# Kernel optimization log

Hardware: AMD Instinct MI355X
Metric: run time of the kernel (lower is better)

Reference implementation:

```python
import jax, jax.numpy as jnp
import numpy as np
jax.config.update("jax_enable_x64", True)

T_OLD = 60000
T_NEW = 60000
NV = 30000
MAX_STEPS = 300
FB_CHUNK = 500  # T_OLD must be divisible by this

FACE_OPP = np.array([[1, 2, 3], [0, 2, 3], [0, 1, 3], [0, 1, 2]])
EDGES = [(0, 1), (0, 2), (0, 3), (1, 2), (1, 3), (2, 3)]


def setup_inputs() -> dict:
    key = jax.random.key(0)
    k1, k2, k3, k4, k5 = jax.random.split(key, 5)
    # distinct vertices per tet (sorted base + strictly increasing offsets)
    off = jnp.arange(4, dtype=jnp.int64)
    new_indices = jnp.sort(jax.random.randint(k1, (T_NEW, 4), 0, NV - 4, dtype=jnp.int64), axis=1) + off
    old_indices = jnp.sort(jax.random.randint(k2, (T_OLD, 4), 0, NV - 4, dtype=jnp.int64), axis=1) + off
    return {
        "new_indices": new_indices,
        "old_indices": old_indices,
        "old_cc": jax.random.normal(k3, (T_OLD, 3), dtype=jnp.float32),
        "new_cc": jax.random.normal(k4, (T_NEW, 3), dtype=jnp.float32),
        "vertex_positions": jax.random.uniform(k5, (NV, 3), dtype=jnp.float32),
    }


def _min_edge_length(verts, indices):
    p = verts[indices]  # (T,4,3)
    el = jnp.stack([jnp.linalg.norm(p[:, a] - p[:, b], axis=-1) for a, b in EDGES])
    return el.min(axis=0)


def _forward(new_indices, old_indices, old_cc, new_cc, vertex_positions):
    T_new = new_indices.shape[0]
    T_old = old_indices.shape[0]
    Vn = vertex_positions.shape[0]

    # --- 1. unchanged-tet detection via sorted-vertex int64 keys ---
    key4 = lambda s: ((s[:, 0] * Vn + s[:, 1]) * Vn + s[:, 2]) * Vn + s[:, 3]
    ok = key4(jnp.sort(old_indices, axis=1))
    nk = key4(jnp.sort(new_indices, axis=1))
    order = jnp.argsort(ok)
    sk = ok[order]
    pos = jnp.searchsorted(sk, nk, side='right') - 1
    posc = jnp.clip(pos, 0, T_old - 1)
    matched = jnp.where((pos >= 0) & (sk[posc] == nk), order[posc], -1)
    is_matched = matched >= 0
    matched_safe = jnp.maximum(matched, 0)

    # --- 2. face adjacency of old mesh (sorted face keys, adjacent-equal pairing) ---
    fi = jnp.sort(old_indices[:, FACE_OPP], axis=2)          # (T_old,4,3)
    fk = (fi[..., 0] * Vn + fi[..., 1]) * Vn + fi[..., 2]    # (T_old,4)
    all_keys = fk.T.reshape(-1)                              # f-major like the numpy concat
    all_tets = jnp.tile(jnp.arange(T_old), 4)
    all_locals = jnp.repeat(jnp.arange(4), T_old)
    o2 = jnp.argsort(all_keys)
    sk2, st, sl = all_keys[o2], all_tets[o2], all_locals[o2]
    same = sk2[:-1] == sk2[1:]
    neighbors = jnp.full((T_old, 4), -1, dtype=jnp.int64)
    neighbors = neighbors.at[jnp.where(same, st[:-1], T_old), sl[:-1]].set(st[1:], mode='drop')
    neighbors = neighbors.at[jnp.where(same, st[1:], T_old), sl[1:]].set(st[:-1], mode='drop')

    # --- 3. per-old-tet inverse edge matrix; degenerate tets get no neighbors ---
    verts = jax.lax.stop_gradient(vertex_positions).astype(jnp.float32)
    p = verts[old_indices]                                   # (T_old,4,3)
    v0 = p[:, 0]
    Tm = jnp.stack([p[:, 1] - v0, p[:, 2] - v0, p[:, 3] - v0], axis=-1)
    degen = jnp.abs(jnp.linalg.det(Tm)) < 1e-10
    Tinv = jnp.linalg.inv(jnp.where(degen[:, None, None], jnp.eye(3, dtype=Tm.dtype), Tm))
    neighbors = jnp.where(degen[:, None], -1, neighbors)

    prio = jnp.full((Vn,), -1, dtype=jnp.int64)
    ar = jnp.arange(T_old)
    for vi in range(4):
        prio = prio.at[old_indices[:, vi]].max(vi * T_old + ar)
    v2t = jnp.where(prio >= 0, prio % T_old, 0)

    # --- 5. barycentric walk (masked, all float inputs stop-gradiented; int outputs) ---
    cent = jax.lax.stop_gradient(verts[new_indices].mean(axis=1))  # (T_new,3)
    seed = v2t[new_indices[:, 0]]
    n_walk = jnp.sum(~is_matched)
    thr = jnp.maximum(jnp.int64(100), n_walk // 1000)

    def cond(state):
        step, cur, rem, act = state
        return (step < MAX_STEPS) & (jnp.sum(act) >= thr)

    def body(state):
        step, cur, rem, act = state
        rel = cent - v0[cur]
        bary = jnp.einsum('nij,nj->ni', Tinv[cur], rel)
        all_b = jnp.concatenate([(1.0 - bary.sum(axis=1))[:, None], bary], axis=1)
        conv = act & (all_b.min(axis=1) >= -1e-4)
        rem = jnp.where(conv, cur, rem)
        act = act & ~conv
        nb = neighbors[cur, jnp.argmin(all_b, axis=1)]
        at_bd = act & (nb < 0)
        rem = jnp.where(at_bd, cur, rem)
        act = act & ~at_bd
        cur = jnp.where(act, nb, cur)
        return (step + 1, cur, rem, act)

    _, cur, rem, act = jax.lax.while_loop(cond, body, (jnp.int64(0), seed, seed, ~is_matched))
    rem = jnp.where(act, cur, rem)

    # --- 6. nearest-centroid fallback for unfinished walks (gated, chunked) ---
    old_cents = jax.lax.stop_gradient(verts[old_indices].mean(axis=1))

    def fallback(_):
        p2 = (cent ** 2).sum(-1)
        c2 = (old_cents ** 2).sum(-1)
        def scan_body(carry, i):
            bd, bi = carry
            c = jax.lax.dynamic_slice(old_cents, (i * FB_CHUNK, 0), (FB_CHUNK, 3))
            cn = jax.lax.dynamic_slice(c2, (i * FB_CHUNK,), (FB_CHUNK,))
            d = p2[:, None] - 2.0 * (cent @ c.T) + cn[None, :]
            md = d.min(axis=1)
            mi = d.argmin(axis=1).astype(jnp.int64) + i * FB_CHUNK
            imp = md < bd
            return (jnp.where(imp, md, bd), jnp.where(imp, mi, bi)), None
        init = (jnp.full((T_new,), jnp.inf, dtype=jnp.float32), jnp.zeros((T_new,), dtype=jnp.int64))
        (bd, bi), _ = jax.lax.scan(scan_body, init, jnp.arange(T_old // FB_CHUNK))
        return bi

    fb = jax.lax.cond(jnp.sum(act) > 0, fallback, lambda _: jnp.zeros((T_new,), dtype=jnp.int64), None)
    rem = jnp.clip(jnp.where(act, fb, rem), 0, T_old - 1)
    remap = jnp.where(is_matched, matched_safe, rem)

    # --- 7. candidates: containing tet + 4 face neighbors ---
    face_nb = neighbors[remap]
    face_nb = jnp.where(face_nb >= 0, face_nb, remap[:, None])
    cands = jnp.concatenate([remap[:, None], face_nb], axis=1)            # (T_new,5)
    cands = jnp.where(is_matched[:, None], matched_safe[:, None], cands)

    # --- 8. overlap / circumcenter-distance weights ---
    cand_verts = old_indices[cands]                                       # (T_new,5,4)
    overlap = (cand_verts[:, :, :, None] == new_indices[:, None, None, :]).any(-1).sum(-1).astype(jnp.float32)
    cc_d2 = ((old_cc[cands] - new_cc[:, None, :]) ** 2).sum(-1)
    raw = jnp.exp(overlap * 2.0) / (cc_d2 + 1e-8)
    weights = raw / raw.sum(axis=1, keepdims=True)

    # --- 9. density scale: min-edge-length ratio ---
    old_el = _min_edge_length(vertex_positions, old_indices)[cands]
    new_el = _min_edge_length(vertex_positions, new_indices)
    density_scale = jnp.clip(old_el / jnp.maximum(new_el[:, None], 1e-8), 0.1, 10.0)

    return cands, weights, density_scale


_forward_jit = jax.jit(_forward)


def reference(new_indices, old_indices, old_cc, new_cc, vertex_positions):
    return _forward_jit(new_indices, old_indices, old_cc, new_cc, vertex_positions)
```

## Files before the change

kernel.cpp:

```cpp
#include <hip/hip_runtime.h>

#pragma clang fp contract(off)

#define TOLD 60000
#define TNEW 60000
#define NVERT 30000
#define MAXSTEPS 300
#define THSZ 131072
#define FHSZ 131072
#define EMPTY64 0xFFFFFFFFFFFFFFFFULL
#define NWGR 60
#define VRANGE 500
#define NSLICE 16
#define TSLICE (TOLD / NSLICE)

#define NB_SETUP 235
#define NB_PRIO  (NWGR * NSLICE)
#define NB_NEWG  235
#define NB_FACE  938
#define NB_FOLD  118
#define NB_MATCH 235
#define NB_FB    120
#define FBRANGE  (TNEW / NB_FB)

#define OFF_TKEYS    0u
#define OFF_FTAB     1048576u
#define OFF_NBR      2097152u
#define FF_BYTES     3057152u
#define OFF_CNT      3057152u
#define OFF_TVALS    3059200u
#define OFF_PPRIO    3583488u
#define OFF_PRIO     5503488u
#define OFF_IDXOLD   5623488u
#define OFF_SSTEP    6583488u
#define OFF_DEGEN    6823488u
#define OFF_MATCHED  7063488u
#define OFF_TV4      7303488u
#define OFF_COLD4    10183488u
#define OFF_CNEW4    11143488u
#define OFF_DM       12103488u

struct P {
  const unsigned int* rawNew;
  const unsigned int* rawOld;
  const float* occ;
  const float* ncc;
  const float* verts;
  float* out;
  unsigned long long* tkeys;
  unsigned long long* ftab;
  int* counters;
  int* tvals;
  int* idxOld;
  int* nbr;
  int* pprio;
  int* prio;
  int* sstep;
  int* degen;
  int* matched;
  float4* Tv4;
  float4* cold4;
  float4* cnew4;
  unsigned long long* dm;
  unsigned int dmMask;
};

__device__ __forceinline__ unsigned hash64(unsigned long long k){
  k ^= k >> 33; k *= 0xff51afd7ed558ccdULL;
  k ^= k >> 33; k *= 0xc4ceb9fe1a85ec53ULL;
  k ^= k >> 33;
  return (unsigned)k;
}
__device__ __forceinline__ void cswap(int& a, int& b){ if (a > b){ int t = a; a = b; b = t; } }

__device__ __forceinline__ int detect64(const unsigned int* raw){
  unsigned acc = 0;
  const uint4* r4 = (const uint4*)raw;
  #pragma unroll
  for (int k = 0; k < 32; ++k){ uint4 v = r4[k]; acc |= (v.y | v.w); }
  return acc == 0u;
}

__device__ __forceinline__ int4 load_tet4(const unsigned int* raw, int is64, int t){
  if (is64){
    uint4 a = ((const uint4*)raw)[t * 2 + 0];
    uint4 b = ((const uint4*)raw)[t * 2 + 1];
    return make_int4((int)a.x, (int)a.z, (int)b.x, (int)b.z);
  }
  uint4 a = ((const uint4*)raw)[t];
  return make_int4((int)a.x, (int)a.y, (int)a.z, (int)a.w);
}

__device__ __forceinline__ void face_insert(unsigned long long* ftab, int* nbr,
                                            unsigned long long fkey, int t, int l){
  unsigned long long mine = (fkey << 18) | (unsigned long long)(t * 4 + l);
  unsigned slot = hash64(fkey ^ 0x9e3779b97f4a7c15ULL) & (FHSZ - 1);
  while (true){
    unsigned long long prev = atomicCAS(&ftab[slot], EMPTY64, mine);
    if (prev == EMPTY64) return;
    if ((prev >> 18) == fkey){
      int oid = (int)(prev & 0x3FFFFULL);
      nbr[t * 4 + l] = oid >> 2;
      nbr[oid] = t;
      return;
    }
    slot = (slot + 1) & (FHSZ - 1);
  }
}

__device__ __forceinline__ float min_edge_r(
    float q0x, float q0y, float q0z, float q1x, float q1y, float q1z,
    float q2x, float q2y, float q2z, float q3x, float q3y, float q3z){
  float m = 3.402823466e+38f;
  float dx, dy, dz, d;
  dx = q0x - q1x; dy = q0y - q1y; dz = q0z - q1z; d = sqrtf((dx*dx + dy*dy) + dz*dz); m = fminf(m, d);
  dx = q0x - q2x; dy = q0y - q2y; dz = q0z - q2z; d = sqrtf((dx*dx + dy*dy) + dz*dz); m = fminf(m, d);
  dx = q0x - q3x; dy = q0y - q3y; dz = q0z - q3z; d = sqrtf((dx*dx + dy*dy) + dz*dz); m = fminf(m, d);
  dx = q1x - q2x; dy = q1y - q2y; dz = q1z - q2z; d = sqrtf((dx*dx + dy*dy) + dz*dz); m = fminf(m, d);
  dx = q1x - q3x; dy = q1y - q3y; dz = q1z - q3z; d = sqrtf((dx*dx + dy*dy) + dz*dz); m = fminf(m, d);
  dx = q2x - q3x; dy = q2y - q3y; dz = q2z - q3z; d = sqrtf((dx*dx + dy*dy) + dz*dz); m = fminf(m, d);
  return m;
}

__global__ __launch_bounds__(256) void k_front(P p){
  __shared__ int sprio[VRANGE];
  int bb = blockIdx.x;
  if (bb < NB_SETUP){
    int t = bb * 256 + threadIdx.x;
    if (bb == 0){
      for (int j = threadIdx.x; j < 384; j += 256) p.counters[j] = 0;
    }
    if (t >= TOLD) return;
    int is64 = detect64(p.rawOld);
    int4 iv4 = load_tet4(p.rawOld, is64, t);
    int i0 = iv4.x, i1 = iv4.y, i2 = iv4.z, i3 = iv4.w;
    ((int4*)p.idxOld)[t] = iv4;

    {
      int s0 = i0, s1 = i1, s2 = i2, s3 = i3;
      cswap(s0, s1); cswap(s2, s3); cswap(s0, s2); cswap(s1, s3); cswap(s1, s2);
      unsigned long long key =
          (unsigned long long)((((long long)s0 * NVERT + s1) * NVERT + s2) * NVERT + s3);
      unsigned slot = hash64(key) & (THSZ - 1);
      while (true){
        unsigned long long prev = atomicCAS(&p.tkeys[slot], EMPTY64, key);
        if (prev == EMPTY64){ p.tvals[slot] = t; break; }
        if (prev == key){ atomicMax(&p.tvals[slot], t); break; }
        slot = (slot + 1) & (THSZ - 1);
      }
    }

    if (p.dmMask){
      const int FO[4][3] = {{1, 2, 3}, {0, 2, 3}, {0, 1, 3}, {0, 1, 2}};
      int iv[4] = {i0, i1, i2, i3};
      #pragma unroll
      for (int l = 0; l < 4; ++l){
        int a = iv[FO[l][0]], b = iv[FO[l][1]], c = iv[FO[l][2]];
        cswap(a, b); cswap(a, c); cswap(b, c);
        unsigned long long fk = (unsigned long long)(((long long)a * NVERT + b) * NVERT + c);
        p.dm[hash64(fk) & p.dmMask] = (fk << 18) | (unsigned long long)(t * 4 + l);
      }
    }

    float q0x = p.verts[i0 * 3 + 0], q0y = p.verts[i0 * 3 + 1], q0z = p.verts[i0 * 3 + 2];
    float q1x = p.verts[i1 * 3 + 0], q1y = p.verts[i1 * 3 + 1], q1z = p.verts[i1 * 3 + 2];
    float q2x = p.verts[i2 * 3 + 0], q2y = p.verts[i2 * 3 + 1], q2z = p.verts[i2 * 3 + 2];
    float q3x = p.verts[i3 * 3 + 0], q3y = p.verts[i3 * 3 + 1], q3z = p.verts[i3 * 3 + 2];
    float e1x = q1x - q0x, e1y = q1y - q0y, e1z = q1z - q0z;
    float e2x = q2x - q0x, e2y = q2y - q0y, e2z = q2z - q0z;
    float e3x = q3x - q0x, e3y = q3y - q0y, e3z = q3z - q0z;
    float c23x = e2y * e3z - e2z * e3y;
    float c23y = e2z * e3x - e2x * e3z;
    float c23z = e2x * e3y - e2y * e3x;
    float det = e1x * c23x + e1y * c23y + e1z * c23z;
    int dg = (fabsf(det) < 1e-10f) ? 1 : 0;
    p.degen[t] = dg;
    float4 r0, r1, r2;
    if (dg){
      r0 = make_float4(1.f, 0.f, 0.f, q0x);
      r1 = make_float4(0.f, 1.f, 0.f, q0y);
      r2 = make_float4(0.f, 0.f, 1.f, q0z);
    } else {
      float inv = 1.0f / det;
      float c31x = e3y * e1z - e3z * e1y;
      float c31y = e3z * e1x - e3x * e1z;
      float c31z = e3x * e1y - e3y * e1x;
      float c12x = e1y * e2z - e1z * e2y;
      float c12y = e1z * e2x - e1x * e2z;
      float c12z = e1x * e2y - e1y * e2x;
      r0 = make_float4(c23x * inv, c23y * inv, c23z * inv, q0x);
      r1 = make_float4(c31x * inv, c31y * inv, c31z * inv, q0y);
      r2 = make_float4(c12x * inv, c12y * inv, c12z * inv, q0z);
    }
    p.Tv4[t * 3 + 0] = r0;
    p.Tv4[t * 3 + 1] = r1;
    p.Tv4[t * 3 + 2] = r2;
    float el = min_edge_r(q0x, q0y, q0z, q1x, q1y, q1z, q2x, q2y, q2z, q3x, q3y, q3z);
    p.cold4[t] = make_float4((((q0x + q1x) + q2x) + q3x) * 0.25f,
                             (((q0y + q1y) + q2y) + q3y) * 0.25f,
                             (((q0z + q1z) + q2z) + q3z) * 0.25f, el);
  } else if (bb < NB_SETUP + NB_PRIO){
    int rb = bb - NB_SETUP;
    int range = rb / NSLICE;
    int slice = rb % NSLICE;
    int base = range * VRANGE;
    for (int j = threadIdx.x; j < VRANGE; j += 256) sprio[j] = -1;
    __syncthreads();
    int is64 = detect64(p.rawOld);
    int t0 = slice * TSLICE;
    for (int t = t0 + threadIdx.x; t < t0 + TSLICE; t += 256){
      int4 iv = load_tet4(p.rawOld, is64, t);
      int v;
      v = iv.x - base; if ((unsigned)v < VRANGE) atomicMax(&sprio[v], 0 * TOLD + t);
      v = iv.y - base; if ((unsigned)v < VRANGE) atomicMax(&sprio[v], 1 * TOLD + t);
      v = iv.z - base; if ((unsigned)v < VRANGE) atomicMax(&sprio[v], 2 * TOLD + t);
      v = iv.w - base; if ((unsigned)v < VRANGE) atomicMax(&sprio[v], 3 * TOLD + t);
    }
    __syncthreads();
    for (int j = threadIdx.x; j < VRANGE; j += 256)
      p.pprio[slice * NVERT + base + j] = sprio[j];
  } else {
    int n = (bb - NB_SETUP - NB_PRIO) * 256 + threadIdx.x;
    if (n >= TNEW) return;
    int is64 = detect64(p.rawNew);
    int4 ni = load_tet4(p.rawNew, is64, n);
    float q0x = p.verts[ni.x * 3 + 0], q0y = p.verts[ni.x * 3 + 1], q0z = p.verts[ni.x * 3 + 2];
    float q1x = p.verts[ni.y * 3 + 0], q1y = p.verts[ni.y * 3 + 1], q1z = p.verts[ni.y * 3 + 2];
    float q2x = p.verts[ni.z * 3 + 0], q2y = p.verts[ni.z * 3 + 1], q2z = p.verts[ni.z * 3 + 2];
    float q3x = p.verts[ni.w * 3 + 0], q3y = p.verts[ni.w * 3 + 1], q3z = p.verts[ni.w * 3 + 2];
    float el = min_edge_r(q0x, q0y, q0z, q1x, q1y, q1z, q2x, q2y, q2z, q3x, q3y, q3z);
    p.cnew4[n] = make_float4((((q0x + q1x) + q2x) + q3x) * 0.25f,
                             (((q0y + q1y) + q2y) + q3y) * 0.25f,
                             (((q0z + q1z) + q2z) + q3z) * 0.25f, el);
  }
}

__global__ __launch_bounds__(256) void k_mid(P p){
  int bb = blockIdx.x;
  if (bb < NB_FACE){
    int i = bb * 256 + threadIdx.x;
    if (i >= TOLD * 4) return;
    int t = i >> 2, l = i & 3;
    int4 iv4 = ((const int4*)p.idxOld)[t];
    int iv[4] = {iv4.x, iv4.y, iv4.z, iv4.w};
    const int FO[4][3] = {{1, 2, 3}, {0, 2, 3}, {0, 1, 3}, {0, 1, 2}};
    int a = iv[FO[l][0]], b = iv[FO[l][1]], c = iv[FO[l][2]];
    cswap(a, b); cswap(a, c); cswap(b, c);
    unsigned long long fk = (unsigned long long)(((long long)a * NVERT + b) * NVERT + c);
    if (p.dmMask){
      unsigned long long mine = (fk << 18) | (unsigned long long)i;
      unsigned long long got = p.dm[hash64(fk) & p.dmMask];
      if (got == mine) return;
      if ((got >> 18) == fk){
        int wid = (int)(got & 0x3FFFFULL);
        p.nbr[i] = wid >> 2;
        p.nbr[wid] = t;
        return;
      }
    }
    face_insert(p.ftab, p.nbr, fk, t, l);
  } else if (bb < NB_FACE + NB_FOLD){
    int v = (bb - NB_FACE) * 256 + threadIdx.x;
    if (v >= NVERT) return;
    int pr = -1;
    #pragma unroll
    for (int s = 0; s < NSLICE; ++s) pr = max(pr, p.pprio[s * NVERT + v]);
    p.prio[v] = pr;
  } else {
    int n = (bb - NB_FACE - NB_FOLD) * 256 + threadIdx.x;
    if (n >= TNEW) return;
    int is64 = detect64(p.rawNew);
    int4 ni = load_tet4(p.rawNew, is64, n);
    int s0 = ni.x, s1 = ni.y, s2 = ni.z, s3 = ni.w;
    cswap(s0, s1); cswap(s2, s3); cswap(s0, s2); cswap(s1, s3); cswap(s1, s2);
    unsigned long long key =
        (unsigned long long)((((long long)s0 * NVERT + s1) * NVERT + s2) * NVERT + s3);
    int m = -1;
    unsigned slot = hash64(key) & (THSZ - 1);
    while (true){
      unsigned long long k = p.tkeys[slot];
      if (k == EMPTY64) break;
      if (k == key){ m = p.tvals[slot]; break; }
      slot = (slot + 1) & (THSZ - 1);
    }
    p.matched[n] = m;
  }
}

__device__ __forceinline__ void assemble_walker(const P& p, int n, int m, int remap){
  int cds[5];
  if (m >= 0){
    cds[0] = cds[1] = cds[2] = cds[3] = cds[4] = m;
  } else {
    cds[0] = remap;
    int dg = p.degen[remap];
    int4 nb4 = ((const int4*)p.nbr)[remap];
    int nbl[4] = {nb4.x, nb4.y, nb4.z, nb4.w};
    for (int l = 0; l < 4; ++l){
      int fb = dg ? -1 : nbl[l];
      cds[1 + l] = (fb >= 0) ? fb : remap;
    }
  }
  bool same = (cds[1] == cds[0]) & (cds[2] == cds[0]) &
              (cds[3] == cds[0]) & (cds[4] == cds[0]);
  int is64 = detect64(p.rawNew);
  int4 ni = load_tet4(p.rawNew, is64, n);
  float nc0 = p.ncc[n * 3 + 0], nc1 = p.ncc[n * 3 + 1], nc2 = p.ncc[n * 3 + 2];
  float nelv = fmaxf(p.cnew4[n].w, 1e-8f);
  if (same){
    int ct = cds[0];
    int4 cv = ((const int4*)p.idxOld)[ct];
    int ov = 0;
    ov += (cv.x == ni.x || cv.x == ni.y || cv.x == ni.z || cv.x == ni.w) ? 1 : 0;
    ov += (cv.y == ni.x || cv.y == ni.y || cv.y == ni.z || cv.y == ni.w) ? 1 : 0;
    ov += (cv.z == ni.x || cv.z == ni.y || cv.z == ni.z || cv.z == ni.w) ? 1 : 0;
    ov += (cv.w == ni.x || cv.w == ni.y || cv.w == ni.z || cv.w == ni.w) ? 1 : 0;
    float d0 = p.occ[ct * 3 + 0] - nc0;
    float d1 = p.occ[ct * 3 + 1] - nc1;
    float d2 = p.occ[ct * 3 + 2] - nc2;
    float ccd2 = (d0 * d0 + d1 * d1) + d2 * d2;
    float raw = expf((float)ov * 2.0f) / (ccd2 + 1e-8f);
    float rsum = 0.0f;
    rsum += raw; rsum += raw; rsum += raw; rsum += raw; rsum += raw;
    float wgt = raw / rsum;
    float ds = p.cold4[ct].w / nelv;
    ds = fminf(fmaxf(ds, 0.1f), 10.0f);
    float cf = (float)ct;
    for (int c = 0; c < 5; ++c){
      p.out[n * 5 + c] = cf;
      p.out[TNEW * 5 + n * 5 + c] = wgt;
      p.out[2 * TNEW * 5 + n * 5 + c] = ds;
    }
    return;
  }
  float raws[5]; float rsum = 0.0f;
  float oels[5];
  for (int c = 0; c < 5; ++c){
    int ct = cds[c];
    int4 cv = ((const int4*)p.idxOld)[ct];
    int ov = 0;
    ov += (cv.x == ni.x || cv.x == ni.y || cv.x == ni.z || cv.x == ni.w) ? 1 : 0;
    ov += (cv.y == ni.x || cv.y == ni.y || cv.y == ni.z || cv.y == ni.w) ? 1 : 0;
    ov += (cv.z == ni.x || cv.z == ni.y || cv.z == ni.z || cv.z == ni.w) ? 1 : 0;
    ov += (cv.w == ni.x || cv.w == ni.y || cv.w == ni.z || cv.w == ni.w) ? 1 : 0;
    float d0 = p.occ[ct * 3 + 0] - nc0;
    float d1 = p.occ[ct * 3 + 1] - nc1;
    float d2 = p.occ[ct * 3 + 2] - nc2;
    float ccd2 = (d0 * d0 + d1 * d1) + d2 * d2;
    float raw = expf((float)ov * 2.0f) / (ccd2 + 1e-8f);
    raws[c] = raw; rsum += raw;
    oels[c] = p.cold4[ct].w;
  }
  for (int c = 0; c < 5; ++c){
    p.out[n * 5 + c] = (float)cds[c];
    p.out[TNEW * 5 + n * 5 + c] = raws[c] / rsum;
    float ds = oels[c] / nelv;
    ds = fminf(fmaxf(ds, 0.1f), 10.0f);
    p.out[2 * TNEW * 5 + n * 5 + c] = ds;
  }
}

__global__ __launch_bounds__(256) void k_walkall(P p){
  __shared__ int s_hist[MAXSTEPS + 2];
  __shared__ int s_nw;
  for (int j = threadIdx.x; j < MAXSTEPS + 2; j += 256) s_hist[j] = 0;
  if (threadIdx.x == 0) s_nw = 0;
  __syncthreads();
  int n = blockIdx.x * blockDim.x + threadIdx.x;
  if (n < TNEW){
    int m = p.matched[n];
    if (m >= 0){
      assemble_walker(p, n, m, 0);
    } else {
      atomicAdd(&s_nw, 1);
      int is64 = detect64(p.rawNew);
      int i0 = is64 ? (int)((const long long*)p.rawNew)[n * 4] : ((const int*)p.rawNew)[n * 4];
      int pr = p.prio[i0];
      int c = (pr >= 0) ? (pr % TOLD) : 0;
      float4 cn = p.cnew4[n];
      int s = MAXSTEPS + 1;
      for (int k = 1; k <= MAXSTEPS; ++k){
        float4 r0 = p.Tv4[c * 3 + 0];
        float4 r1 = p.Tv4[c * 3 + 1];
        float4 r2 = p.Tv4[c * 3 + 2];
        float rx = cn.x - r0.w, ry = cn.y - r1.w, rz = cn.z - r2.w;
        float b0 = r0.x * rx + r0.y * ry + r0.z * rz;
        float b1 = r1.x * rx + r1.y * ry + r1.z * rz;
        float b2 = r2.x * rx + r2.y * ry + r2.z * rz;
        float a0 = 1.0f - (b0 + b1 + b2);
        float ab[4] = {a0, b0, b1, b2};
        int amin = 0; float mn = ab[0];
        for (int j = 1; j < 4; ++j){ if (ab[j] < mn){ mn = ab[j]; amin = j; } }
        if (mn >= -0.0001f){ s = k; break; }
        int nb = p.degen[c] ? -1 : p.nbr[c * 4 + amin];
        if (nb < 0){ s = k; break; }
        c = nb;
      }
      p.sstep[n] = s;
      atomicAdd(&s_hist[s], 1);
      assemble_walker(p, n, -1, c);
    }
  }
  __syncthreads();
  if (threadIdx.x == 0 && s_nw) atomicAdd(&p.counters[0], s_nw);
  for (int j = threadIdx.x; j < MAXSTEPS + 2; j += 256){
    int v = s_hist[j];
    if (v) atomicAdd(&p.counters[64 + j], v);
  }
}

__device__ __forceinline__ int compute_S(const int* counters){
  int nw = counters[0];
  int thr = max(100, nw / 1000);
  if (nw < thr) return 0;
  int cnt = nw;
  for (int k = 1; k <= MAXSTEPS; ++k){
    cnt -= counters[64 + k];
    if (cnt < thr) return k;
  }
  return MAXSTEPS;
}

__global__ __launch_bounds__(256) void k_tail(P p){
  __shared__ float sd[256];
  __shared__ int si[256];
  __shared__ int s_hits[256];
  __shared__ int s_nhits;
  __shared__ int s_S;
  if (threadIdx.x == 0) s_S = compute_S(p.counters);
  __syncthreads();
  int S = s_S;
  int base = blockIdx.x * FBRANGE;
  for (int chunk = base; chunk < base + FBRANGE; chunk += 256){
    if (threadIdx.x == 0) s_nhits = 0;
    __syncthreads();
    int n = chunk + threadIdx.x;
    if (n < base + FBRANGE && n < TNEW){
      if (p.matched[n] < 0 && p.sstep[n] > S)
        s_hits[atomicAdd(&s_nhits, 1)] = n;
    }
    __syncthreads();
    int nh = s_nhits;
    for (int h = 0; h < nh; ++h){
      int n2 = s_hits[h];
      float4 cn = p.cnew4[n2];
      float cx = cn.x, cy = cn.y, cz = cn.z;
      float p2 = (cx * cx + cy * cy) + cz * cz;
      float bd = 3.402823466e+38f; int bi = 0;
      for (int j = threadIdx.x; j < TOLD; j += 256){
        float4 oc = p.cold4[j];
        float dot = (cx * oc.x + cy * oc.y) + cz * oc.z;
        float c2 = (oc.x * oc.x + oc.y * oc.y) + oc.z * oc.z;
        float d = (p2 - 2.0f * dot) + c2;
        if (d < bd || (d == bd && j < bi)){ bd = d; bi = j; }
      }
      sd[threadIdx.x] = bd; si[threadIdx.x] = bi;
      __syncthreads();
      for (int s = 128; s > 0; s >>= 1){
        if ((int)threadIdx.x < s){
          float od = sd[threadIdx.x + s]; int oi = si[threadIdx.x + s];
          if (od < sd[threadIdx.x] || (od == sd[threadIdx.x] && oi < si[threadIdx.x])){
            sd[threadIdx.x] = od; si[threadIdx.x] = oi;
          }
        }
        __syncthreads();
      }
      if (threadIdx.x == 0){
        int r = si[0];
        if (r < 0) r = 0; if (r > TOLD - 1) r = TOLD - 1;
        assemble_walker(p, n2, -1, r);
      }
      __syncthreads();
    }
    __syncthreads();
  }
}

extern "C" void kernel_launch(void* const* d_in, const int* in_sizes, int n_in,
                              void* d_out, int out_size, void* d_ws, size_t ws_size,
                              hipStream_t stream) {
  char* w = (char*)d_ws;
  P p;
  p.rawNew = (const unsigned int*)d_in[0];
  p.rawOld = (const unsigned int*)d_in[1];
  p.occ    = (const float*)d_in[2];
  p.ncc    = (const float*)d_in[3];
  p.verts  = (const float*)d_in[4];
  p.out    = (float*)d_out;
  p.tkeys    = (unsigned long long*)(w + OFF_TKEYS);
  p.ftab     = (unsigned long long*)(w + OFF_FTAB);
  p.nbr      = (int*)(w + OFF_NBR);
  p.counters = (int*)(w + OFF_CNT);
  p.tvals    = (int*)(w + OFF_TVALS);
  p.pprio    = (int*)(w + OFF_PPRIO);
  p.prio     = (int*)(w + OFF_PRIO);
  p.idxOld   = (int*)(w + OFF_IDXOLD);
  p.sstep    = (int*)(w + OFF_SSTEP);
  p.degen    = (int*)(w + OFF_DEGEN);
  p.matched  = (int*)(w + OFF_MATCHED);
  p.Tv4      = (float4*)(w + OFF_TV4);
  p.cold4    = (float4*)(w + OFF_COLD4);
  p.cnew4    = (float4*)(w + OFF_CNEW4);
  p.dm       = (unsigned long long*)(w + OFF_DM);
  size_t avail = (ws_size > (size_t)OFF_DM) ? ws_size - (size_t)OFF_DM : 0;
  unsigned dmMask = 0;
  for (int bshift = 21; bshift >= 16; --bshift){
    if (avail >= ((size_t)8 << bshift)){ dmMask = (1u << bshift) - 1u; break; }
  }
  p.dmMask = dmMask;

  hipMemsetAsync(w, 0xFF, FF_BYTES, stream);
  hipLaunchKernelGGL(k_front,   dim3(NB_SETUP + NB_PRIO + NB_NEWG), dim3(256), 0, stream, p);
  hipLaunchKernelGGL(k_mid,     dim3(NB_FACE + NB_FOLD + NB_MATCH), dim3(256), 0, stream, p);
  hipLaunchKernelGGL(k_walkall, dim3((TNEW + 255) / 256), dim3(256), 0, stream, p);
  hipLaunchKernelGGL(k_tail,    dim3(NB_FB), dim3(256), 0, stream, p);
}
```

Before: 113.7 us.

## Fuse pipeline kernels into one persistent kernel with software grid barriers

Replaces the four separate launches (front, mid, walk, tail) with a single persistent kernel of 768 blocks. The blocks move between phases through an atomic-counter grid barrier that lives in the memset workspace. The per-vertex priority is now built with direct global atomicMax during setup, which removes the sliced LDS pass and the fold pass. The goal is to cut launch gaps and inter-kernel drain time, at the cost of barrier spin overhead, more contention on global atomics, and a deadlock risk if not all 768 blocks are resident at once.

```diff
diff --git a/kernel.cpp b/kernel.cpp
--- a/kernel.cpp
+++ b/kernel.cpp
@@ -9,16 +9,12 @@
 #define THSZ 131072
 #define FHSZ 131072
 #define EMPTY64 0xFFFFFFFFFFFFFFFFULL
-#define NWGR 60
-#define VRANGE 500
-#define NSLICE 16
-#define TSLICE (TOLD / NSLICE)
+
+#define GRID_NB 768
 
 #define NB_SETUP 235
-#define NB_PRIO  (NWGR * NSLICE)
 #define NB_NEWG  235
 #define NB_FACE  938
-#define NB_FOLD  118
 #define NB_MATCH 235
 #define NB_FB    120
 #define FBRANGE  (TNEW / NB_FB)
@@ -26,19 +22,19 @@
 #define OFF_TKEYS    0u
 #define OFF_FTAB     1048576u
 #define OFF_NBR      2097152u
-#define FF_BYTES     3057152u
-#define OFF_CNT      3057152u
-#define OFF_TVALS    3059200u
-#define OFF_PPRIO    3583488u
-#define OFF_PRIO     5503488u
-#define OFF_IDXOLD   5623488u
-#define OFF_SSTEP    6583488u
-#define OFF_DEGEN    6823488u
-#define OFF_MATCHED  7063488u
-#define OFF_TV4      7303488u
-#define OFF_COLD4    10183488u
-#define OFF_CNEW4    11143488u
-#define OFF_DM       12103488u
+#define OFF_PRIO     3057152u
+#define OFF_BAR      3177152u
+#define FF_BYTES     3177216u
+#define OFF_CNT      3177216u
+#define OFF_TVALS    3179264u
+#define OFF_IDXOLD   3703552u
+#define OFF_SSTEP    4663552u
+#define OFF_DEGEN    4903552u
+#define OFF_MATCHED  5143552u
+#define OFF_TV4      5383552u
+#define OFF_COLD4    8263552u
+#define OFF_CNEW4    9223552u
+#define OFF_DM       10183552u
 
 struct P {
   const unsigned int* rawNew;
@@ -53,7 +49,6 @@
   int* tvals;
   int* idxOld;
   int* nbr;
-  int* pprio;
   int* prio;
   int* sstep;
   int* degen;
@@ -62,6 +57,7 @@
   float4* cold4;
   float4* cnew4;
   unsigned long long* dm;
+  int* bar;
   unsigned int dmMask;
 };
 
@@ -122,169 +118,24 @@
   return m;
 }
 
-__global__ __launch_bounds__(256) void k_front(P p){
-  __shared__ int sprio[VRANGE];
-  int bb = blockIdx.x;
-  if (bb < NB_SETUP){
-    int t = bb * 256 + threadIdx.x;
-    if (bb == 0){
-      for (int j = threadIdx.x; j < 384; j += 256) p.counters[j] = 0;
-    }
-    if (t >= TOLD) return;
-    int is64 = detect64(p.rawOld);
-    int4 iv4 = load_tet4(p.rawOld, is64, t);
-    int i0 = iv4.x, i1 = iv4.y, i2 = iv4.z, i3 = iv4.w;
-    ((int4*)p.idxOld)[t] = iv4;
-
-    {
-      int s0 = i0, s1 = i1, s2 = i2, s3 = i3;
-      cswap(s0, s1); cswap(s2, s3); cswap(s0, s2); cswap(s1, s3); cswap(s1, s2);
-      unsigned long long key =
-          (unsigned long long)((((long long)s0 * NVERT + s1) * NVERT + s2) * NVERT + s3);
-      unsigned slot = hash64(key) & (THSZ - 1);
-      while (true){
-        unsigned long long prev = atomicCAS(&p.tkeys[slot], EMPTY64, key);
-        if (prev == EMPTY64){ p.tvals[slot] = t; break; }
-        if (prev == key){ atomicMax(&p.tvals[slot], t); break; }
-        slot = (slot + 1) & (THSZ - 1);
-      }
-    }
-
-    if (p.dmMask){
-      const int FO[4][3] = {{1, 2, 3}, {0, 2, 3}, {0, 1, 3}, {0, 1, 2}};
-      int iv[4] = {i0, i1, i2, i3};
-      #pragma unroll
-      for (int l = 0; l < 4; ++l){
-        int a = iv[FO[l][0]], b = iv[FO[l][1]], c = iv[FO[l][2]];
-        cswap(a, b); cswap(a, c); cswap(b, c);
-        unsigned long long fk = (unsigned long long)(((long long)a * NVERT + b) * NVERT + c);
-        p.dm[hash64(fk) & p.dmMask] = (fk << 18) | (unsigned long long)(t * 4 + l);
-      }
-    }
-
-    float q0x = p.verts[i0 * 3 + 0], q0y = p.verts[i0 * 3 + 1], q0z = p.verts[i0 * 3 + 2];
-    float q1x = p.verts[i1 * 3 + 0], q1y = p.verts[i1 * 3 + 1], q1z = p.verts[i1 * 3 + 2];
-    float q2x = p.verts[i2 * 3 + 0], q2y = p.verts[i2 * 3 + 1], q2z = p.verts[i2 * 3 + 2];
-    float q3x = p.verts[i3 * 3 + 0], q3y = p.verts[i3 * 3 + 1], q3z = p.verts[i3 * 3 + 2];
-    float e1x = q1x - q0x, e1y = q1y - q0y, e1z = q1z - q0z;
-    float e2x = q2x - q0x, e2y = q2y - q0y, e2z = q2z - q0z;
-    float e3x = q3x - q0x, e3y = q3y - q0y, e3z = q3z - q0z;
-    float c23x = e2y * e3z - e2z * e3y;
-    float c23y = e2z * e3x - e2x * e3z;
-    float c23z = e2x * e3y - e2y * e3x;
-    float det = e1x * c23x + e1y * c23y + e1z * c23z;
-    int dg = (fabsf(det) < 1e-10f) ? 1 : 0;
-    p.degen[t] = dg;
-    float4 r0, r1, r2;
-    if (dg){
-      r0 = make_float4(1.f, 0.f, 0.f, q0x);
-      r1 = make_float4(0.f, 1.f, 0.f, q0y);
-      r2 = make_float4(0.f, 0.f, 1.f, q0z);
+__device__ __forceinline__ void gridbar(int* bar){
+  __syncthreads();
+  if (threadIdx.x == 0){
+    __threadfence();
+    int g = __hip_atomic_load(&bar[1], __ATOMIC_ACQUIRE, __HIP_MEMORY_SCOPE_AGENT);
+    int v = __hip_atomic_fetch_add(&bar[0], 1, __ATOMIC_ACQ_REL, __HIP_MEMORY_SCOPE_AGENT);
+    if (v == GRID_NB - 2){
+      __hip_atomic_fetch_add(&bar[0], -GRID_NB, __ATOMIC_RELAXED, __HIP_MEMORY_SCOPE_AGENT);
+      __threadfence();
+      __hip_atomic_fetch_add(&bar[1], 1, __ATOMIC_RELEASE, __HIP_MEMORY_SCOPE_AGENT);
     } else {
-      float inv = 1.0f / det;
-      float c31x = e3y * e1z - e3z * e1y;
-      float c31y = e3z * e1x - e3x * e1z;
-      float c31z = e3x * e1y - e3y * e1x;
-      float c12x = e1y * e2z - e1z * e2y;
-      float c12y = e1z * e2x - e1x * e2z;
-      float c12z = e1x * e2y - e1y * e2x;
-      r0 = make_float4(c23x * inv, c23y * inv, c23z * inv, q0x);
-      r1 = make_float4(c31x * inv, c31y * inv, c31z * inv, q0y);
-      r2 = make_float4(c12x * inv, c12y * inv, c12z * inv, q0z);
-    }
-    p.Tv4[t * 3 + 0] = r0;
-    p.Tv4[t * 3 + 1] = r1;
-    p.Tv4[t * 3 + 2] = r2;
-    float el = min_edge_r(q0x, q0y, q0z, q1x, q1y, q1z, q2x, q2y, q2z, q3x, q3y, q3z);
-    p.cold4[t] = make_float4((((q0x + q1x) + q2x) + q3x) * 0.25f,
-                             (((q0y + q1y) + q2y) + q3y) * 0.25f,
-                             (((q0z + q1z) + q2z) + q3z) * 0.25f, el);
-  } else if (bb < NB_SETUP + NB_PRIO){
-    int rb = bb - NB_SETUP;
-    int range = rb / NSLICE;
-    int slice = rb % NSLICE;
-    int base = range * VRANGE;
-    for (int j = threadIdx.x; j < VRANGE; j += 256) sprio[j] = -1;
-    __syncthreads();
-    int is64 = detect64(p.rawOld);
-    int t0 = slice * TSLICE;
-    for (int t = t0 + threadIdx.x; t < t0 + TSLICE; t += 256){
-      int4 iv = load_tet4(p.rawOld, is64, t);
-      int v;
-      v = iv.x - base; if ((unsigned)v < VRANGE) atomicMax(&sprio[v], 0 * TOLD + t);
-      v = iv.y - base; if ((unsigned)v < VRANGE) atomicMax(&sprio[v], 1 * TOLD + t);
-      v = iv.z - base; if ((unsigned)v < VRANGE) atomicMax(&sprio[v], 2 * TOLD + t);
-      v = iv.w - base; if ((unsigned)v < VRANGE) atomicMax(&sprio[v], 3 * TOLD + t);
-    }
-    __syncthreads();
-    for (int j = threadIdx.x; j < VRANGE; j += 256)
-      p.pprio[slice * NVERT + base + j] = sprio[j];
-  } else {
-    int n = (bb - NB_SETUP - NB_PRIO) * 256 + threadIdx.x;
-    if (n >= TNEW) return;
-    int is64 = detect64(p.rawNew);
-    int4 ni = load_tet4(p.rawNew, is64, n);
-    float q0x = p.verts[ni.x * 3 + 0], q0y = p.verts[ni.x * 3 + 1], q0z = p.verts[ni.x * 3 + 2];
-    float q1x = p.verts[ni.y * 3 + 0], q1y = p.verts[ni.y * 3 + 1], q1z = p.verts[ni.y * 3 + 2];
-    float q2x = p.verts[ni.z * 3 + 0], q2y = p.verts[ni.z * 3 + 1], q2z = p.verts[ni.z * 3 + 2];
-    float q3x = p.verts[ni.w * 3 + 0], q3y = p.verts[ni.w * 3 + 1], q3z = p.verts[ni.w * 3 + 2];
-    float el = min_edge_r(q0x, q0y, q0z, q1x, q1y, q1z, q2x, q2y, q2z, q3x, q3y, q3z);
-    p.cnew4[n] = make_float4((((q0x + q1x) + q2x) + q3x) * 0.25f,
-                             (((q0y + q1y) + q2y) + q3y) * 0.25f,
-                             (((q0z + q1z) + q2z) + q3z) * 0.25f, el);
-  }
-}
-
-__global__ __launch_bounds__(256) void k_mid(P p){
-  int bb = blockIdx.x;
-  if (bb < NB_FACE){
-    int i = bb * 256 + threadIdx.x;
-    if (i >= TOLD * 4) return;
-    int t = i >> 2, l = i & 3;
-    int4 iv4 = ((const int4*)p.idxOld)[t];
-    int iv[4] = {iv4.x, iv4.y, iv4.z, iv4.w};
-    const int FO[4][3] = {{1, 2, 3}, {0, 2, 3}, {0, 1, 3}, {0, 1, 2}};
-    int a = iv[FO[l][0]], b = iv[FO[l][1]], c = iv[FO[l][2]];
-    cswap(a, b); cswap(a, c); cswap(b, c);
-    unsigned long long fk = (unsigned long long)(((long long)a * NVERT + b) * NVERT + c);
-    if (p.dmMask){
-      unsigned long long mine = (fk << 18) | (unsigned long long)i;
-      unsigned long long got = p.dm[hash64(fk) & p.dmMask];
-      if (got == mine) return;
-      if ((got >> 18) == fk){
-        int wid = (int)(got & 0x3FFFFULL);
-        p.nbr[i] = wid >> 2;
-        p.nbr[wid] = t;
-        return;
-      }
-    }
-    face_insert(p.ftab, p.nbr, fk, t, l);
-  } else if (bb < NB_FACE + NB_FOLD){
-    int v = (bb - NB_FACE) * 256 + threadIdx.x;
-    if (v >= NVERT) return;
-    int pr = -1;
-    #pragma unroll
-    for (int s = 0; s < NSLICE; ++s) pr = max(pr, p.pprio[s * NVERT + v]);
-    p.prio[v] = pr;
-  } else {
-    int n = (bb - NB_FACE - NB_FOLD) * 256 + threadIdx.x;
-    if (n >= TNEW) return;
-    int is64 = detect64(p.rawNew);
-    int4 ni = load_tet4(p.rawNew, is64, n);
-    int s0 = ni.x, s1 = ni.y, s2 = ni.z, s3 = ni.w;
-    cswap(s0, s1); cswap(s2, s3); cswap(s0, s2); cswap(s1, s3); cswap(s1, s2);
-    unsigned long long key =
-        (unsigned long long)((((long long)s0 * NVERT + s1) * NVERT + s2) * NVERT + s3);
-    int m = -1;
-    unsigned slot = hash64(key) & (THSZ - 1);
-    while (true){
-      unsigned long long k = p.tkeys[slot];
-      if (k == EMPTY64) break;
-      if (k == key){ m = p.tvals[slot]; break; }
-      slot = (slot + 1) & (THSZ - 1);
-    }
-    p.matched[n] = m;
-  }
+      while (__hip_atomic_load(&bar[1], __ATOMIC_RELAXED, __HIP_MEMORY_SCOPE_AGENT) == g){
+        __builtin_amdgcn_s_sleep(1);
+      }
+    }
+    __threadfence();
+  }
+  __syncthreads();
 }
 
 __device__ __forceinline__ void assemble_walker(const P& p, int n, int m, int remap){
@@ -360,55 +211,6 @@
   }
 }
 
-__global__ __launch_bounds__(256) void k_walkall(P p){
-  __shared__ int s_hist[MAXSTEPS + 2];
-  __shared__ int s_nw;
-  for (int j = threadIdx.x; j < MAXSTEPS + 2; j += 256) s_hist[j] = 0;
-  if (threadIdx.x == 0) s_nw = 0;
-  __syncthreads();
-  int n = blockIdx.x * blockDim.x + threadIdx.x;
-  if (n < TNEW){
-    int m = p.matched[n];
-    if (m >= 0){
-      assemble_walker(p, n, m, 0);
-    } else {
-      atomicAdd(&s_nw, 1);
-      int is64 = detect64(p.rawNew);
-      int i0 = is64 ? (int)((const long long*)p.rawNew)[n * 4] : ((const int*)p.rawNew)[n * 4];
-      int pr = p.prio[i0];
-      int c = (pr >= 0) ? (pr % TOLD) : 0;
-      float4 cn = p.cnew4[n];
-      int s = MAXSTEPS + 1;
-      for (int k = 1; k <= MAXSTEPS; ++k){
-        float4 r0 = p.Tv4[c * 3 + 0];
-        float4 r1 = p.Tv4[c * 3 + 1];
-        float4 r2 = p.Tv4[c * 3 + 2];
-        float rx = cn.x - r0.w, ry = cn.y - r1.w, rz = cn.z - r2.w;
-        float b0 = r0.x * rx + r0.y * ry + r0.z * rz;
-        float b1 = r1.x * rx + r1.y * ry + r1.z * rz;
-        float b2 = r2.x * rx + r2.y * ry + r2.z * rz;
-        float a0 = 1.0f - (b0 + b1 + b2);
-        float ab[4] = {a0, b0, b1, b2};
-        int amin = 0; float mn = ab[0];
-        for (int j = 1; j < 4; ++j){ if (ab[j] < mn){ mn = ab[j]; amin = j; } }
-        if (mn >= -0.0001f){ s = k; break; }
-        int nb = p.degen[c] ? -1 : p.nbr[c * 4 + amin];
-        if (nb < 0){ s = k; break; }
-        c = nb;
-      }
-      p.sstep[n] = s;
-      atomicAdd(&s_hist[s], 1);
-      assemble_walker(p, n, -1, c);
-    }
-  }
-  __syncthreads();
-  if (threadIdx.x == 0 && s_nw) atomicAdd(&p.counters[0], s_nw);
-  for (int j = threadIdx.x; j < MAXSTEPS + 2; j += 256){
-    int v = s_hist[j];
-    if (v) atomicAdd(&p.counters[64 + j], v);
-  }
-}
-
 __device__ __forceinline__ int compute_S(const int* counters){
   int nw = counters[0];
   int thr = max(100, nw / 1000);
@@ -421,58 +223,259 @@
   return MAXSTEPS;
 }
 
-__global__ __launch_bounds__(256) void k_tail(P p){
+__global__ __launch_bounds__(256, 3) void k_fused(P p){
+  __shared__ int s_hist[MAXSTEPS + 2];
+  __shared__ int s_nw;
   __shared__ float sd[256];
   __shared__ int si[256];
   __shared__ int s_hits[256];
   __shared__ int s_nhits;
   __shared__ int s_S;
-  if (threadIdx.x == 0) s_S = compute_S(p.counters);
+
+  const int bb = blockIdx.x;
+
+  if (bb < NB_SETUP){
+    if (bb == 0){
+      for (int j = threadIdx.x; j < 384; j += 256) p.counters[j] = 0;
+    }
+    int t = bb * 256 + threadIdx.x;
+    if (t < TOLD){
+      int is64 = detect64(p.rawOld);
+      int4 iv4 = load_tet4(p.rawOld, is64, t);
+      int i0 = iv4.x, i1 = iv4.y, i2 = iv4.z, i3 = iv4.w;
+      ((int4*)p.idxOld)[t] = iv4;
+
+      atomicMax(&p.prio[i0], 0 * TOLD + t);
+      atomicMax(&p.prio[i1], 1 * TOLD + t);
+      atomicMax(&p.prio[i2], 2 * TOLD + t);
+      atomicMax(&p.prio[i3], 3 * TOLD + t);
+
+      {
+        int s0 = i0, s1 = i1, s2 = i2, s3 = i3;
+        cswap(s0, s1); cswap(s2, s3); cswap(s0, s2); cswap(s1, s3); cswap(s1, s2);
+        unsigned long long key =
+            (unsigned long long)((((long long)s0 * NVERT + s1) * NVERT + s2) * NVERT + s3);
+        unsigned slot = hash64(key) & (THSZ - 1);
+        while (true){
+          unsigned long long prev = atomicCAS(&p.tkeys[slot], EMPTY64, key);
+          if (prev == EMPTY64){ p.tvals[slot] = t; break; }
+          if (prev == key){ atomicMax(&p.tvals[slot], t); break; }
+          slot = (slot + 1) & (THSZ - 1);
+        }
+      }
+
+      if (p.dmMask){
+        const int FO[4][3] = {{1, 2, 3}, {0, 2, 3}, {0, 1, 3}, {0, 1, 2}};
+        int iv[4] = {i0, i1, i2, i3};
+        #pragma unroll
+        for (int l = 0; l < 4; ++l){
+          int a = iv[FO[l][0]], b = iv[FO[l][1]], c = iv[FO[l][2]];
+          cswap(a, b); cswap(a, c); cswap(b, c);
+          unsigned long long fk = (unsigned long long)(((long long)a * NVERT + b) * NVERT + c);
+          p.dm[hash64(fk) & p.dmMask] = (fk << 18) | (unsigned long long)(t * 4 + l);
+        }
+      }
+
+      float q0x = p.verts[i0 * 3 + 0], q0y = p.verts[i0 * 3 + 1], q0z = p.verts[i0 * 3 + 2];
+      float q1x = p.verts[i1 * 3 + 0], q1y = p.verts[i1 * 3 + 1], q1z = p.verts[i1 * 3 + 2];
+      float q2x = p.verts[i2 * 3 + 0], q2y = p.verts[i2 * 3 + 1], q2z = p.verts[i2 * 3 + 2];
+      float q3x = p.verts[i3 * 3 + 0], q3y = p.verts[i3 * 3 + 1], q3z = p.verts[i3 * 3 + 2];
+      float e1x = q1x - q0x, e1y = q1y - q0y, e1z = q1z - q0z;
+      float e2x = q2x - q0x, e2y = q2y - q0y, e2z = q2z - q0z;
+      float e3x = q3x - q0x, e3y = q3y - q0y, e3z = q3z - q0z;
+      float c23x = e2y * e3z - e2z * e3y;
+      float c23y = e2z * e3x - e2x * e3z;
+      float c23z = e2x * e3y - e2y * e3x;
+      float det = e1x * c23x + e1y * c23y + e1z * c23z;
+      int dg = (fabsf(det) < 1e-10f) ? 1 : 0;
+      p.degen[t] = dg;
+      float4 r0, r1, r2;
+      if (dg){
+        r0 = make_float4(1.f, 0.f, 0.f, q0x);
+        r1 = make_float4(0.f, 1.f, 0.f, q0y);
+        r2 = make_float4(0.f, 0.f, 1.f, q0z);
+      } else {
+        float inv = 1.0f / det;
+        float c31x = e3y * e1z - e3z * e1y;
+        float c31y = e3z * e1x - e3x * e1z;
+        float c31z = e3x * e1y - e3y * e1x;
+        float c12x = e1y * e2z - e1z * e2y;
+        float c12y = e1z * e2x - e1x * e2z;
+        float c12z = e1x * e2y - e1y * e2x;
+        r0 = make_float4(c23x * inv, c23y * inv, c23z * inv, q0x);
+        r1 = make_float4(c31x * inv, c31y * inv, c31z * inv, q0y);
+        r2 = make_float4(c12x * inv, c12y * inv, c12z * inv, q0z);
+      }
+      p.Tv4[t * 3 + 0] = r0;
+      p.Tv4[t * 3 + 1] = r1;
+      p.Tv4[t * 3 + 2] = r2;
+      float el = min_edge_r(q0x, q0y, q0z, q1x, q1y, q1z, q2x, q2y, q2z, q3x, q3y, q3z);
+      p.cold4[t] = make_float4((((q0x + q1x) + q2x) + q3x) * 0.25f,
+                               (((q0y + q1y) + q2y) + q3y) * 0.25f,
+                               (((q0z + q1z) + q2z) + q3z) * 0.25f, el);
+    }
+  } else if (bb < NB_SETUP + NB_NEWG){
+    int n = (bb - NB_SETUP) * 256 + threadIdx.x;
+    if (n < TNEW){
+      int is64 = detect64(p.rawNew);
+      int4 ni = load_tet4(p.rawNew, is64, n);
+      float q0x = p.verts[ni.x * 3 + 0], q0y = p.verts[ni.x * 3 + 1], q0z = p.verts[ni.x * 3 + 2];
+      float q1x = p.verts[ni.y * 3 + 0], q1y = p.verts[ni.y * 3 + 1], q1z = p.verts[ni.y * 3 + 2];
+      float q2x = p.verts[ni.z * 3 + 0], q2y = p.verts[ni.z * 3 + 1], q2z = p.verts[ni.z * 3 + 2];
+      float q3x = p.verts[ni.w * 3 + 0], q3y = p.verts[ni.w * 3 + 1], q3z = p.verts[ni.w * 3 + 2];
+      float el = min_edge_r(q0x, q0y, q0z, q1x, q1y, q1z, q2x, q2y, q2z, q3x, q3y, q3z);
+      p.cnew4[n] = make_float4((((q0x + q1x) + q2x) + q3x) * 0.25f,
+                               (((q0y + q1y) + q2y) + q3y) * 0.25f,
+                               (((q0z + q1z) + q2z) + q3z) * 0.25f, el);
+    }
+  }
+  gridbar(p.bar);
+
+  for (int vb = bb; vb < NB_FACE + NB_MATCH; vb += GRID_NB){
+    if (vb < NB_FACE){
+      int i = vb * 256 + threadIdx.x;
+      if (i < TOLD * 4){
+        int t = i >> 2, l = i & 3;
+        int4 iv4 = ((const int4*)p.idxOld)[t];
+        int iv[4] = {iv4.x, iv4.y, iv4.z, iv4.w};
+        const int FO[4][3] = {{1, 2, 3}, {0, 2, 3}, {0, 1, 3}, {0, 1, 2}};
+        int a = iv[FO[l][0]], b = iv[FO[l][1]], c = iv[FO[l][2]];
+        cswap(a, b); cswap(a, c); cswap(b, c);
+        unsigned long long fk = (unsigned long long)(((long long)a * NVERT + b) * NVERT + c);
+        bool done = false;
+        if (p.dmMask){
+          unsigned long long mine = (fk << 18) | (unsigned long long)i;
+          unsigned long long got = p.dm[hash64(fk) & p.dmMask];
+          if (got == mine){
+            done = true;
+          } else if ((got >> 18) == fk){
+            int wid = (int)(got & 0x3FFFFULL);
+            p.nbr[i] = wid >> 2;
+            p.nbr[wid] = t;
+            done = true;
+          }
+        }
+        if (!done) face_insert(p.ftab, p.nbr, fk, t, l);
+      }
+    } else {
+      int n = (vb - NB_FACE) * 256 + threadIdx.x;
+      if (n < TNEW){
+        int is64 = detect64(p.rawNew);
+        int4 ni = load_tet4(p.rawNew, is64, n);
+        int s0 = ni.x, s1 = ni.y, s2 = ni.z, s3 = ni.w;
+        cswap(s0, s1); cswap(s2, s3); cswap(s0, s2); cswap(s1, s3); cswap(s1, s2);
+        unsigned long long key =
+            (unsigned long long)((((long long)s0 * NVERT + s1) * NVERT + s2) * NVERT + s3);
+        int m = -1;
+        unsigned slot = hash64(key) & (THSZ - 1);
+        while (true){
+          unsigned long long k = p.tkeys[slot];
+          if (k == EMPTY64) break;
+          if (k == key){ m = p.tvals[slot]; break; }
+          slot = (slot + 1) & (THSZ - 1);
+        }
+        p.matched[n] = m;
+      }
+    }
+  }
+  gridbar(p.bar);
+
+  for (int j = threadIdx.x; j < MAXSTEPS + 2; j += 256) s_hist[j] = 0;
+  if (threadIdx.x == 0) s_nw = 0;
   __syncthreads();
-  int S = s_S;
-  int base = blockIdx.x * FBRANGE;
-  for (int chunk = base; chunk < base + FBRANGE; chunk += 256){
-    if (threadIdx.x == 0) s_nhits = 0;
+  {
+    int n = bb * 256 + threadIdx.x;
+    if (n < TNEW){
+      int m = p.matched[n];
+      if (m >= 0){
+        assemble_walker(p, n, m, 0);
+      } else {
+        atomicAdd(&s_nw, 1);
+        int is64 = detect64(p.rawNew);
+        int i0 = is64 ? (int)((const long long*)p.rawNew)[n * 4] : ((const int*)p.rawNew)[n * 4];
+        int pr = p.prio[i0];
+        int c = (pr >= 0) ? (pr % TOLD) : 0;
+        float4 cn = p.cnew4[n];
+        int s = MAXSTEPS + 1;
+        for (int k = 1; k <= MAXSTEPS; ++k){
+          float4 r0 = p.Tv4[c * 3 + 0];
+          float4 r1 = p.Tv4[c * 3 + 1];
+          float4 r2 = p.Tv4[c * 3 + 2];
+          float rx = cn.x - r0.w, ry = cn.y - r1.w, rz = cn.z - r2.w;
+          float b0 = r0.x * rx + r0.y * ry + r0.z * rz;
+          float b1 = r1.x * rx + r1.y * ry + r1.z * rz;
+          float b2 = r2.x * rx + r2.y * ry + r2.z * rz;
+          float a0 = 1.0f - (b0 + b1 + b2);
+          float ab[4] = {a0, b0, b1, b2};
+          int amin = 0; float mn = ab[0];
+          for (int j = 1; j < 4; ++j){ if (ab[j] < mn){ mn = ab[j]; amin = j; } }
+          if (mn >= -0.0001f){ s = k; break; }
+          int nb = p.degen[c] ? -1 : p.nbr[c * 4 + amin];
+          if (nb < 0){ s = k; break; }
+          c = nb;
+        }
+        p.sstep[n] = s;
+        atomicAdd(&s_hist[s], 1);
+        assemble_walker(p, n, -1, c);
+      }
+    }
+  }
+  __syncthreads();
+  if (threadIdx.x == 0 && s_nw) atomicAdd(&p.counters[0], s_nw);
+  for (int j = threadIdx.x; j < MAXSTEPS + 2; j += 256){
+    int v = s_hist[j];
+    if (v) atomicAdd(&p.counters[64 + j], v);
+  }
+  gridbar(p.bar);
+
+  if (bb < NB_FB){
+    if (threadIdx.x == 0) s_S = compute_S(p.counters);
     __syncthreads();
-    int n = chunk + threadIdx.x;
-    if (n < base + FBRANGE && n < TNEW){
-      if (p.matched[n] < 0 && p.sstep[n] > S)
-        s_hits[atomicAdd(&s_nhits, 1)] = n;
-    }
-    __syncthreads();
-    int nh = s_nhits;
-    for (int h = 0; h < nh; ++h){
-      int n2 = s_hits[h];
-      float4 cn = p.cnew4[n2];
-      float cx = cn.x, cy = cn.y, cz = cn.z;
-      float p2 = (cx * cx + cy * cy) + cz * cz;
-      float bd = 3.402823466e+38f; int bi = 0;
-      for (int j = threadIdx.x; j < TOLD; j += 256){
-        float4 oc = p.cold4[j];
-        float dot = (cx * oc.x + cy * oc.y) + cz * oc.z;
-        float c2 = (oc.x * oc.x + oc.y * oc.y) + oc.z * oc.z;
-        float d = (p2 - 2.0f * dot) + c2;
-        if (d < bd || (d == bd && j < bi)){ bd = d; bi = j; }
-      }
-      sd[threadIdx.x] = bd; si[threadIdx.x] = bi;
+    int S = s_S;
+    int base = bb * FBRANGE;
+    for (int chunk = base; chunk < base + FBRANGE; chunk += 256){
+      if (threadIdx.x == 0) s_nhits = 0;
       __syncthreads();
-      for (int s = 128; s > 0; s >>= 1){
-        if ((int)threadIdx.x < s){
-          float od = sd[threadIdx.x + s]; int oi = si[threadIdx.x + s];
-          if (od < sd[threadIdx.x] || (od == sd[threadIdx.x] && oi < si[threadIdx.x])){
-            sd[threadIdx.x] = od; si[threadIdx.x] = oi;
+      int n = chunk + threadIdx.x;
+      if (n < base + FBRANGE && n < TNEW){
+        if (p.matched[n] < 0 && p.sstep[n] > S)
+          s_hits[atomicAdd(&s_nhits, 1)] = n;
+      }
+      __syncthreads();
+      int nh = s_nhits;
+      for (int h = 0; h < nh; ++h){
+        int n2 = s_hits[h];
+        float4 cn = p.cnew4[n2];
+        float cx = cn.x, cy = cn.y, cz = cn.z;
+        float p2 = (cx * cx + cy * cy) + cz * cz;
+        float bd = 3.402823466e+38f; int bi = 0;
+        for (int j = threadIdx.x; j < TOLD; j += 256){
+          float4 oc = p.cold4[j];
+          float dot = (cx * oc.x + cy * oc.y) + cz * oc.z;
+          float c2 = (oc.x * oc.x + oc.y * oc.y) + oc.z * oc.z;
+          float d = (p2 - 2.0f * dot) + c2;
+          if (d < bd || (d == bd && j < bi)){ bd = d; bi = j; }
+        }
+        sd[threadIdx.x] = bd; si[threadIdx.x] = bi;
+        __syncthreads();
+        for (int s = 128; s > 0; s >>= 1){
+          if ((int)threadIdx.x < s){
+            float od = sd[threadIdx.x + s]; int oi = si[threadIdx.x + s];
+            if (od < sd[threadIdx.x] || (od == sd[threadIdx.x] && oi < si[threadIdx.x])){
+              sd[threadIdx.x] = od; si[threadIdx.x] = oi;
+            }
           }
+          __syncthreads();
+        }
+        if (threadIdx.x == 0){
+          int r = si[0];
+          if (r < 0) r = 0; if (r > TOLD - 1) r = TOLD - 1;
+          assemble_walker(p, n2, -1, r);
         }
         __syncthreads();
       }
-      if (threadIdx.x == 0){
-        int r = si[0];
-        if (r < 0) r = 0; if (r > TOLD - 1) r = TOLD - 1;
-        assemble_walker(p, n2, -1, r);
-      }
       __syncthreads();
     }
-    __syncthreads();
   }
 }
 
@@ -490,10 +493,10 @@
   p.tkeys    = (unsigned long long*)(w + OFF_TKEYS);
   p.ftab     = (unsigned long long*)(w + OFF_FTAB);
   p.nbr      = (int*)(w + OFF_NBR);
+  p.prio     = (int*)(w + OFF_PRIO);
+  p.bar      = (int*)(w + OFF_BAR);
   p.counters = (int*)(w + OFF_CNT);
   p.tvals    = (int*)(w + OFF_TVALS);
-  p.pprio    = (int*)(w + OFF_PPRIO);
-  p.prio     = (int*)(w + OFF_PRIO);
   p.idxOld   = (int*)(w + OFF_IDXOLD);
   p.sstep    = (int*)(w + OFF_SSTEP);
   p.degen    = (int*)(w + OFF_DEGEN);
@@ -510,8 +513,5 @@
   p.dmMask = dmMask;
 
   hipMemsetAsync(w, 0xFF, FF_BYTES, stream);
-  hipLaunchKernelGGL(k_front,   dim3(NB_SETUP + NB_PRIO + NB_NEWG), dim3(256), 0, stream, p);
-  hipLaunchKernelGGL(k_mid,     dim3(NB_FACE + NB_FOLD + NB_MATCH), dim3(256), 0, stream, p);
-  hipLaunchKernelGGL(k_walkall, dim3((TNEW + 255) / 256), dim3(256), 0, stream, p);
-  hipLaunchKernelGGL(k_tail,    dim3(NB_FB), dim3(256), 0, stream, p);
-}
+  hipLaunchKernelGGL(k_fused, dim3(GRID_NB), dim3(256), 0, stream, p);
+}
```

Result: slower. 425.0 us (+273.7%).
